# Kernel tuning notes

Measured on AMD Instinct MI355X. Metric: run time of the kernel, lower is better.

## Reference

```python
import jax, jax.numpy as jnp
import numpy as np

EPS = 1e-5

def rmsnorm(x, w, eps=EPS):
    # torch-style RMSNorm: x / rms(x) * weight
    return x * jax.lax.rsqrt(jnp.mean(x * x, axis=-1, keepdims=True) + eps) * w

def setup_inputs() -> dict:
    key = jax.random.key(0)
    k1, k2 = jax.random.split(key)
    B, T, D, Q, K = 8, 1024, 1024, 8, 4096
    d = D // Q
    x = jax.random.normal(k1, (B, T, D), dtype=jnp.float32)
    codebooks = jax.random.normal(k2, (Q, K, d), dtype=jnp.float32)
    input_norm_w = jnp.ones((D,), dtype=jnp.float32)
    output_norm_w = jnp.ones((D,), dtype=jnp.float32)
    return {"x": x, "codebooks": codebooks,
            "input_norm_w": input_norm_w, "output_norm_w": output_norm_w}

def reference(x, codebooks, input_norm_w, output_norm_w):
    B, T, D = x.shape
    Q, K, d = codebooks.shape
    xn = rmsnorm(x, input_norm_w)
    xq = xn.reshape(B, T, Q, d)  # split hidden into Q sub-vectors
    # squared euclidean distances (argmin equal to cdist argmin)
    x2 = jnp.sum(xq * xq, axis=-1, keepdims=True)          # [B,T,Q,1]
    c2 = jnp.sum(codebooks * codebooks, axis=-1)           # [Q,K]
    xc = jnp.einsum('btqd,qkd->btqk', xq, codebooks)       # [B,T,Q,K]
    d2 = x2 - 2.0 * xc + c2[None, None]                    # [B,T,Q,K]
    idx = jnp.argmin(d2, axis=-1)                          # [B,T,Q] int
    # gather nearest code per quantizer: equivalent of stacked embedding lookups
    quant = codebooks[jnp.arange(Q)[None, None, :], idx]   # [B,T,Q,d]
    quant = quant.reshape(B, T, D)
    out = rmsnorm(quant, output_norm_w)
    return out, idx
```

## Files before the change

kernel.cpp:

```cpp
#include <hip/hip_runtime.h>
#include <math.h>
#include <float.h>

#define Q_     8
#define K_     4096
#define dd_    128
#define D_     1024
#define ROWS   8192
#define NCHUNK 64
#define TAU    0.04f

typedef __attribute__((ext_vector_type(8))) _Float16 f16x8;
typedef __attribute__((ext_vector_type(4))) float f32x4;
typedef __attribute__((ext_vector_type(4))) unsigned int u32x4;

typedef const __attribute__((address_space(1))) unsigned int* gas_p;
typedef __attribute__((address_space(3))) unsigned int* las_p;

__device__ inline unsigned f2u(float x) { union { float f; unsigned u; } v; v.f = x; return v.u; }
__device__ inline float u2f(unsigned x) { union { unsigned u; float f; } v; v.u = x; return v.f; }
__device__ inline unsigned short f2h(float x) {
    union { _Float16 h; unsigned short u; } v; v.h = (_Float16)x; return v.u;
}
__device__ inline unsigned umin_(unsigned a, unsigned b) { return a < b ? a : b; }
__device__ inline unsigned umax_(unsigned a, unsigned b) { return a > b ? a : b; }
__device__ inline unsigned fflip(float x) {
    unsigned u = f2u(x);
    return (u & 0x80000000u) ? ~u : (u | 0x80000000u);
}
__device__ inline unsigned long long shfl_xor_u64(unsigned long long v, int m) {
    unsigned lo = (unsigned)v, hi = (unsigned)(v >> 32);
    lo = __shfl_xor(lo, m, 64);
    hi = __shfl_xor(hi, m, 64);
    return ((unsigned long long)hi << 32) | lo;
}
__device__ inline unsigned dec_k(unsigned v, int e) {
    unsigned tg = v & 0x7Fu;
    return ((tg >> 1) << 6) | (((unsigned)e >> 4) << 5) | ((tg & 1u) << 4) | ((unsigned)e & 15u);
}

__global__ void k_prep(const float* __restrict__ cb, const float* __restrict__ x,
                       const float* __restrict__ w, float* __restrict__ xn,
                       unsigned short* __restrict__ panels, float* __restrict__ c2h,
                       float* __restrict__ x2h, int* __restrict__ cntF, int* __restrict__ cntS) {
    const int bid = blockIdx.x, t = threadIdx.x;
    if (bid == 0 && t == 0) { *cntF = 0; *cntS = 0; }
    if (bid < NCHUNK * Q_) {
        int c = bid & 63, q = bid >> 6;
        const float* src = cb + ((size_t)q * K_ + c * 64) * dd_;
        unsigned short* dst = panels + (size_t)(q * NCHUNK + c) * 8192;
        #pragma unroll
        for (int i = 0; i < 4; i++) {
            int sid = i * 256 + t;
            int n = sid >> 4, j = sid & 15;
            const float* sp = src + n * dd_ + j * 8;
            f32x4 v0 = *(const f32x4*)sp;
            f32x4 v1 = *(const f32x4*)(sp + 4);
            float xs[8] = {v0.x, v0.y, v0.z, v0.w, v1.x, v1.y, v1.z, v1.w};
            unsigned short hb[8];
            float ss = 0.0f;
            #pragma unroll
            for (int e = 0; e < 8; e++) {
                float xv = -xs[e];
                ss = fmaf(xv, xv, ss);
                hb[e] = f2h(xv);
            }
            int slot = j ^ (n & 15);
            u32x4 H;
            H.x = (unsigned)hb[0] | ((unsigned)hb[1] << 16);
            H.y = (unsigned)hb[2] | ((unsigned)hb[3] << 16);
            H.z = (unsigned)hb[4] | ((unsigned)hb[5] << 16);
            H.w = (unsigned)hb[6] | ((unsigned)hb[7] << 16);
            *(u32x4*)&dst[(n * 16 + slot) * 8] = H;
            ss += __shfl_xor(ss, 1, 64);
            ss += __shfl_xor(ss, 2, 64);
            ss += __shfl_xor(ss, 4, 64);
            ss += __shfl_xor(ss, 8, 64);
            if (j == 0) c2h[q * K_ + c * 64 + n] = 0.5f * ss;
        }
    } else {
        int row = bid - NCHUNK * Q_;
        const float4 v = *(const float4*)(x + (size_t)row * D_ + t * 4);
        float ss = v.x * v.x + v.y * v.y + v.z * v.z + v.w * v.w;
        #pragma unroll
        for (int o = 32; o > 0; o >>= 1) ss += __shfl_xor(ss, o, 64);
        __shared__ float acc[4];
        if ((t & 63) == 0) acc[t >> 6] = ss;
        __syncthreads();
        float tot = (acc[0] + acc[1]) + (acc[2] + acc[3]);
        float sc  = 1.0f / sqrtf(tot * (1.0f / D_) + 1e-5f);
        const float4 wv = *(const float4*)(w + t * 4);
        float4 o;
        o.x = v.x * sc * wv.x; o.y = v.y * sc * wv.y;
        o.z = v.z * sc * wv.z; o.w = v.w * sc * wv.w;
        *(float4*)(xn + (size_t)row * D_ + t * 4) = o;
        float so = o.x * o.x + o.y * o.y + o.z * o.z + o.w * o.w;
        so += __shfl_xor(so, 1, 64);
        so += __shfl_xor(so, 2, 64);
        so += __shfl_xor(so, 4, 64);
        so += __shfl_xor(so, 8, 64);
        so += __shfl_xor(so, 16, 64);
        if ((t & 31) == 0) x2h[row * Q_ + (t >> 5)] = 0.5f * so;
    }
}

#define STAGE(CN) do {                                                                   \
    const char* src_ = (const char*)(panels + panq + (size_t)(CN) * 8192);               \
    char* stg_ = smem + ((CN) & 1) * 16384;                                              \
    _Pragma("unroll")                                                                    \
    for (int i_ = 0; i_ < 4; i_++) {                                                     \
        int boff_ = i_ * 4096 + t * 16;                                                  \
        __builtin_amdgcn_global_load_lds((gas_p)(src_ + boff_), (las_p)(stg_ + boff_),   \
                                         16, 0, 0);                                      \
    }                                                                                    \
} while (0)

__launch_bounds__(256, 4)
__global__ void k_dist(const float* __restrict__ xn, const unsigned short* __restrict__ panels,
                       const float* __restrict__ c2h, const float* __restrict__ x2h,
                       int* __restrict__ idxi, float* __restrict__ idxf,
                       int* __restrict__ listF, int* __restrict__ cntF,
                       int* __restrict__ srl, int* __restrict__ cntS,
                       unsigned long long* __restrict__ resc,
                       unsigned char* __restrict__ fbm) {
    __shared__ char smem[32768];

    const int t    = threadIdx.x;
    const int lane = t & 63, wave = t >> 6;
    const int wm = wave >> 1, wn = wave & 1;
    const int col = lane & 15, quad = lane >> 4;
    const int q = blockIdx.y;
    const int row0 = blockIdx.x * 64;

    f16x8 ah[2][4];
    #pragma unroll
    for (int mt = 0; mt < 2; mt++) {
        #pragma unroll
        for (int kt = 0; kt < 4; kt++) {
            const float* ap = xn + (size_t)(row0 + wm * 32 + mt * 16 + col) * D_
                              + q * dd_ + kt * 32 + quad * 8;
            f32x4 v0 = *(const f32x4*)ap;
            f32x4 v1 = *(const f32x4*)(ap + 4);
            #pragma unroll
            for (int e = 0; e < 8; e++) {
                float xv = (e < 4) ? v0[e] : v1[e - 4];
                ah[mt][kt][e] = (_Float16)xv;
            }
        }
    }

    f32x4 x2v[2];
    #pragma unroll
    for (int mt = 0; mt < 2; mt++)
        #pragma unroll
        for (int r = 0; r < 4; r++)
            x2v[mt][r] = x2h[(size_t)(row0 + wm * 32 + mt * 16 + quad * 4 + r) * Q_ + q];

    unsigned m1[8], m2[8], m3[8];
    #pragma unroll
    for (int i = 0; i < 8; i++) { m1[i] = 0xFFFFFFFFu; m2[i] = 0xFFFFFFFFu; m3[i] = 0xFFFFFFFFu; }

    const size_t panq = (size_t)q * NCHUNK * 8192;
    const float* c2hq = c2h + q * K_;

    STAGE(0);
    float ch0 = c2hq[wn * 32 + col];
    float ch1 = c2hq[wn * 32 + col + 16];

    for (int c = 0; c < NCHUNK; c++) {
        __syncthreads();
        if (c + 1 < NCHUNK) STAGE(c + 1);
        float ch0n = 0.0f, ch1n = 0.0f;
        if (c + 1 < NCHUNK) {
            ch0n = c2hq[(c + 1) * 64 + wn * 32 + col];
            ch1n = c2hq[(c + 1) * 64 + wn * 32 + col + 16];
        }
        const char* cbuf = smem + (c & 1) * 16384;

        f32x4 acc[2][2];
        #pragma unroll
        for (int mt = 0; mt < 2; mt++) {
            acc[mt][0] = x2v[mt] + ch0;
            acc[mt][1] = x2v[mt] + ch1;
        }

        #pragma unroll
        for (int kt = 0; kt < 4; kt++) {
            const int sw = ((quad + kt * 4) ^ col) * 16;
            const int a0 = (wn * 32 + col) * 256 + sw;
            const int a1 = a0 + 4096;
            f16x8 b0 = *(const f16x8*)(cbuf + a0);
            f16x8 b1 = *(const f16x8*)(cbuf + a1);
            #pragma unroll
            for (int mt = 0; mt < 2; mt++) {
                acc[mt][0] = __builtin_amdgcn_mfma_f32_16x16x32_f16(ah[mt][kt], b0, acc[mt][0], 0, 0, 0);
                acc[mt][1] = __builtin_amdgcn_mfma_f32_16x16x32_f16(ah[mt][kt], b1, acc[mt][1], 0, 0, 0);
            }
        }

        const unsigned tg0 = (unsigned)(c << 1), tg1 = tg0 | 1u;
        #pragma unroll
        for (int mt = 0; mt < 2; mt++) {
            #pragma unroll
            for (int r = 0; r < 4; r++) {
                const int sl = mt * 4 + r;
                unsigned p0 = (f2u(acc[mt][0][r]) & 0xFFFFFF80u) | tg0;
                unsigned p1 = (f2u(acc[mt][1][r]) & 0xFFFFFF80u) | tg1;
                unsigned pmin = umin_(p0, p1), pmax = umax_(p0, p1);
                unsigned a1m = umax_(m1[sl], pmin);
                unsigned a2m = umin_(m2[sl], pmax);
                unsigned a4m = umax_(m2[sl], pmax);
                m1[sl] = umin_(m1[sl], pmin);
                m2[sl] = umin_(a1m, a2m);
                unsigned a3m = umax_(a1m, a2m);
                m3[sl] = umin_(umin_(a3m, a4m), m3[sl]);
            }
        }
        ch0 = ch0n; ch1 = ch1n;
    }

    __syncthreads();
    unsigned* rm1 = (unsigned*)smem;
    unsigned* rm2 = (unsigned*)(smem + 8448);
    unsigned* rm3 = (unsigned*)(smem + 16896);
    #pragma unroll
    for (int mt = 0; mt < 2; mt++) {
        #pragma unroll
        for (int r = 0; r < 4; r++) {
            int sl = mt * 4 + r;
            int row_l = wm * 32 + mt * 16 + quad * 4 + r;
            int e = wn * 16 + col;
            rm1[row_l * 33 + e] = m1[sl];
            rm2[row_l * 33 + e] = m2[sl];
            rm3[row_l * 33 + e] = m3[sl];
        }
    }
    __syncthreads();
    if (t < 64) {
        unsigned b1 = 0xFFFFFFFFu;
        int be = 0;
        for (int e = 0; e < 32; e++) {
            unsigned v1 = rm1[t * 33 + e];
            if (v1 < b1) { b1 = v1; be = e; }
        }
        float thr = u2f(b1 & 0xFFFFFF80u) + TAU;
        int ns = 0, fb = 0;
        unsigned long long candpack = 0;
        for (int e = 0; e < 32; e++) {
            unsigned v1 = rm1[t * 33 + e];
            unsigned v2 = rm2[t * 33 + e];
            unsigned v3 = rm3[t * 33 + e];
            if (u2f(v3 & 0xFFFFFF80u) < thr) fb = 1;
            if (e != be && u2f(v1 & 0xFFFFFF80u) < thr) {
                if (ns < 5) candpack |= (unsigned long long)dec_k(v1, e) << (12 * ns);
                ns++;
            }
            if (u2f(v2 & 0xFFFFFF80u) < thr) {
                if (ns < 5) candpack |= (unsigned long long)dec_k(v2, e) << (12 * ns);
                ns++;
            }
        }
        if (ns > 5) fb = 1;
        unsigned k1 = dec_k(b1, be);
        int item = (row0 + t) * Q_ + q;
        idxi[item] = (int)k1;
        idxf[item] = (float)k1;
        fbm[item] = (unsigned char)fb;
        if (fb) {
            resc[item] = 0xFFFFFFFFFFFFFFFFull;
            int p = atomicAdd(cntF, 1);
            listF[p] = item;
        } else if (ns > 0) {
            int p = atomicAdd(cntS, 1);
            int* e8 = srl + (size_t)p * 8;
            e8[0] = item; e8[1] = ns + 1; e8[2] = (int)k1;
            for (int i = 0; i < ns; i++)
                e8[3 + i] = (int)((candpack >> (12 * i)) & 0xFFFu);
        }
    }
}

__global__ void k_rescue(const float* __restrict__ xn, const float* __restrict__ cb,
                         const float* __restrict__ c2h, const int* __restrict__ listF,
                         const int* __restrict__ cntF, const int* __restrict__ srl,
                         const int* __restrict__ cntS,
                         unsigned long long* __restrict__ resc,
                         int* __restrict__ idxi, float* __restrict__ idxf) {
    __shared__ float xq[dd_];
    __shared__ unsigned long long kshare[8];
    const int t = threadIdx.x;
    if (blockIdx.x < 2048) {
        const int n = *cntF;
        const int seg = blockIdx.x & 7;
        for (int ii = blockIdx.x >> 3; ii < n; ii += 256) {
            __syncthreads();
            int item = listF[ii];
            int rg = item >> 3, q = item & 7;
            if (t < dd_) xq[t] = xn[(size_t)rg * D_ + q * dd_ + t];
            __syncthreads();
            unsigned long long best = 0xFFFFFFFFFFFFFFFFull;
            #pragma unroll
            for (int i = 0; i < 2; i++) {
                int k = seg * 512 + i * 256 + t;
                const float* cp = cb + ((size_t)q * K_ + k) * dd_;
                float dot = 0.0f;
                #pragma unroll 8
                for (int d = 0; d < dd_; d += 4) {
                    f32x4 cv = *(const f32x4*)(cp + d);
                    dot = fmaf(cv.x, xq[d],     dot);
                    dot = fmaf(cv.y, xq[d + 1], dot);
                    dot = fmaf(cv.z, xq[d + 2], dot);
                    dot = fmaf(cv.w, xq[d + 3], dot);
                }
                float s = c2h[q * K_ + k] - dot;
                unsigned long long key = ((unsigned long long)fflip(s) << 32) | (unsigned)k;
                best = best < key ? best : key;
            }
            #pragma unroll
            for (int o = 32; o > 0; o >>= 1) {
                unsigned long long other = shfl_xor_u64(best, o);
                best = best < other ? best : other;
            }
            if ((t & 63) == 0) kshare[t >> 6] = best;
            __syncthreads();
            if (t == 0) {
                unsigned long long b = kshare[0];
                b = b < kshare[1] ? b : kshare[1];
                b = b < kshare[2] ? b : kshare[2];
                b = b < kshare[3] ? b : kshare[3];
                atomicMin(&resc[item], b);
            }
        }
    } else {
        const int n = *cntS;
        for (int ii = (int)blockIdx.x - 2048; ii < n; ii += 2048) {
            __syncthreads();
            const int* e = srl + (size_t)ii * 8;
            int item = e[0], nc = e[1];
            int rg = item >> 3, q = item & 7;
            if (t < dd_) xq[t] = xn[(size_t)rg * D_ + q * dd_ + t];
            __syncthreads();
            int g = t >> 5, l = t & 31;
            unsigned long long key = 0xFFFFFFFFFFFFFFFFull;
            if (g < nc) {
                int k = e[2 + g];
                const float* cp = cb + ((size_t)q * K_ + k) * dd_ + l * 4;
                f32x4 cv = *(const f32x4*)cp;
                float dot = cv.x * xq[l * 4]     + cv.y * xq[l * 4 + 1]
                          + cv.z * xq[l * 4 + 2] + cv.w * xq[l * 4 + 3];
                dot += __shfl_xor(dot, 16, 64);
                dot += __shfl_xor(dot, 8, 64);
                dot += __shfl_xor(dot, 4, 64);
                dot += __shfl_xor(dot, 2, 64);
                dot += __shfl_xor(dot, 1, 64);
                float s = c2h[q * K_ + k] - dot;
                key = ((unsigned long long)fflip(s) << 32) | (unsigned)k;
            }
            if (l == 0) kshare[g] = key;
            __syncthreads();
            if (t == 0) {
                unsigned long long b = kshare[0];
                #pragma unroll
                for (int gg = 1; gg < 8; gg++) b = b < kshare[gg] ? b : kshare[gg];
                int k = (int)(unsigned)(b & 0xFFFFFFFFull);
                idxi[item] = k;
                idxf[item] = (float)k;
            }
        }
    }
}

__global__ void k_out(const float* __restrict__ cb, const int* __restrict__ idx_i,
                      const unsigned long long* __restrict__ resc,
                      const unsigned char* __restrict__ fbm,
                      const float* __restrict__ w, float* __restrict__ out,
                      float* __restrict__ idxf) {
    int row = blockIdx.x;
    int t   = threadIdx.x;
    __shared__ int   sidx[Q_];
    __shared__ float acc[4];
    if (t < Q_) {
        int item = row * Q_ + t;
        int k = idx_i[item];
        if (fbm[item]) {
            k = (int)(unsigned)(resc[item] & 0xFFFFFFFFull);
            idxf[item] = (float)k;
        }
        sidx[t] = k;
    }
    __syncthreads();
    int col = t * 4;
    int q   = col >> 7;
    int dc  = col & 127;
    const float4 v = *(const float4*)(cb + ((size_t)q * K_ + sidx[q]) * dd_ + dc);
    float ss = v.x * v.x + v.y * v.y + v.z * v.z + v.w * v.w;
    #pragma unroll
    for (int o = 32; o > 0; o >>= 1) ss += __shfl_xor(ss, o, 64);
    if ((t & 63) == 0) acc[t >> 6] = ss;
    __syncthreads();
    float tot = (acc[0] + acc[1]) + (acc[2] + acc[3]);
    float sc  = 1.0f / sqrtf(tot * (1.0f / D_) + 1e-5f);
    const float4 wv = *(const float4*)(w + col);
    float4 o;
    o.x = v.x * sc * wv.x; o.y = v.y * sc * wv.y;
    o.z = v.z * sc * wv.z; o.w = v.w * sc * wv.w;
    *(float4*)(out + (size_t)row * D_ + col) = o;
}

extern "C" void kernel_launch(void* const* d_in, const int* in_sizes, int n_in,
                              void* d_out, int out_size, void* d_ws, size_t ws_size,
                              hipStream_t stream) {
    const float* x     = (const float*)d_in[0];
    const float* cb    = (const float*)d_in[1];
    const float* w_in  = (const float*)d_in[2];
    const float* w_out = (const float*)d_in[3];

    float* out  = (float*)d_out;
    float* idxf = out + (size_t)ROWS * D_;

    unsigned short* panels = (unsigned short*)d_ws;
    float* c2h  = (float*)((char*)d_ws + (8u << 20));
    float* x2h  = c2h + Q_ * K_;
    unsigned long long* resc = (unsigned long long*)(x2h + (size_t)ROWS * Q_);
    int*   idxi = (int*)(resc + (size_t)ROWS * Q_);
    int*   listF = idxi + ROWS * Q_;
    int*   srl  = listF + ROWS * Q_;
    unsigned char* fbm = (unsigned char*)(srl + (size_t)ROWS * Q_ * 8);
    int*   cntF = (int*)(fbm + ROWS * Q_);
    int*   cntS = cntF + 1;

    k_prep  <<<dim3(NCHUNK * Q_ + ROWS), 256, 0, stream>>>(cb, x, w_in, out, panels, c2h, x2h, cntF, cntS);
    k_dist  <<<dim3(ROWS / 64, Q_),      256, 0, stream>>>(out, panels, c2h, x2h, idxi, idxf, listF, cntF, srl, cntS, resc, fbm);
    k_rescue<<<dim3(4096),               256, 0, stream>>>(out, cb, c2h, listF, cntF, srl, cntS, resc, idxi, idxf);
    k_out   <<<dim3(ROWS),               256, 0, stream>>>(cb, idxi, resc, fbm, w_out, out, idxf);
}
```

Baseline: 217.0 us.

## Give each wave its own LDS double buffer and drop block barriers in distance loop

Restructures the distance kernel's main loop. Previously all four waves shared a block-wide double buffer of 64-code chunks and hit a __syncthreads every iteration. Now each wave stages its own 16-code half-chunk into a private LDS region and waits on it with explicit s_waitcnt vmcnt, so block-level barriers go away. Chunks become 32 codes, which doubles the iteration count and adjusts the tag encoding, and the top-3 update is simplified to one candidate per step. The cost is that waves sharing a column half each load the same panel data, so global/L2 traffic doubles, and correctness depends on the hand-written vmcnt count.

```diff
diff --git a/kernel.cpp b/kernel.cpp
--- a/kernel.cpp
+++ b/kernel.cpp
@@ -7,7 +7,7 @@
 #define dd_    128
 #define D_     1024
 #define ROWS   8192
-#define NCHUNK 64
+#define NCHUNK 128
 #define TAU    0.04f
 
 typedef __attribute__((ext_vector_type(8))) _Float16 f16x8;
@@ -35,8 +35,7 @@
     return ((unsigned long long)hi << 32) | lo;
 }
 __device__ inline unsigned dec_k(unsigned v, int e) {
-    unsigned tg = v & 0x7Fu;
-    return ((tg >> 1) << 6) | (((unsigned)e >> 4) << 5) | ((tg & 1u) << 4) | ((unsigned)e & 15u);
+    return (v & 0x7Fu) * 32u + (unsigned)e;
 }
 
 __global__ void k_prep(const float* __restrict__ cb, const float* __restrict__ x,
@@ -45,10 +44,10 @@
                        float* __restrict__ x2h, int* __restrict__ cntF, int* __restrict__ cntS) {
     const int bid = blockIdx.x, t = threadIdx.x;
     if (bid == 0 && t == 0) { *cntF = 0; *cntS = 0; }
-    if (bid < NCHUNK * Q_) {
+    if (bid < 64 * Q_) {
         int c = bid & 63, q = bid >> 6;
         const float* src = cb + ((size_t)q * K_ + c * 64) * dd_;
-        unsigned short* dst = panels + (size_t)(q * NCHUNK + c) * 8192;
+        unsigned short* dst = panels + ((size_t)q * 64 + c) * 8192;
         #pragma unroll
         for (int i = 0; i < 4; i++) {
             int sid = i * 256 + t;
@@ -79,7 +78,7 @@
             if (j == 0) c2h[q * K_ + c * 64 + n] = 0.5f * ss;
         }
     } else {
-        int row = bid - NCHUNK * Q_;
+        int row = bid - 64 * Q_;
         const float4 v = *(const float4*)(x + (size_t)row * D_ + t * 4);
         float ss = v.x * v.x + v.y * v.y + v.z * v.z + v.w * v.w;
         #pragma unroll
@@ -104,14 +103,42 @@
     }
 }
 
-#define STAGE(CN) do {                                                                   \
-    const char* src_ = (const char*)(panels + panq + (size_t)(CN) * 8192);               \
-    char* stg_ = smem + ((CN) & 1) * 16384;                                              \
+#define ITER(C, CHCUR, CHNXT) do {                                                       \
+    if ((C) + 1 < NCHUNK) {                                                              \
+        const char* s_ = (const char*)(panels + panq + (size_t)((C) + 1) * 4096)         \
+                         + wn * 4096;                                                    \
+        char* d_ = mybuf + (((C) + 1) & 1) * 4096;                                       \
+        _Pragma("unroll")                                                                \
+        for (int i_ = 0; i_ < 4; i_++) {                                                 \
+            int o_ = i_ * 1024 + lane * 16;                                              \
+            __builtin_amdgcn_global_load_lds((gas_p)(s_ + o_), (las_p)(d_ + o_),         \
+                                             16, 0, 0);                                  \
+        }                                                                                \
+        CHNXT = c2hq[((C) + 1) * 32 + wn * 16 + col];                                    \
+        asm volatile("s_waitcnt vmcnt(5)" ::: "memory");                                 \
+    } else {                                                                             \
+        asm volatile("s_waitcnt vmcnt(0)" ::: "memory");                                 \
+    }                                                                                    \
+    const char* cb_ = mybuf + ((C) & 1) * 4096;                                          \
+    f32x4 acc0 = x2v0 + (CHCUR);                                                         \
+    f32x4 acc1 = x2v1 + (CHCUR);                                                         \
     _Pragma("unroll")                                                                    \
-    for (int i_ = 0; i_ < 4; i_++) {                                                     \
-        int boff_ = i_ * 4096 + t * 16;                                                  \
-        __builtin_amdgcn_global_load_lds((gas_p)(src_ + boff_), (las_p)(stg_ + boff_),   \
-                                         16, 0, 0);                                      \
+    for (int kt_ = 0; kt_ < 4; kt_++) {                                                  \
+        f16x8 b_ = *(const f16x8*)(cb_ + col * 256 + (((quad + kt_ * 4) ^ col) * 16));   \
+        acc0 = __builtin_amdgcn_mfma_f32_16x16x32_f16(ah[0][kt_], b_, acc0, 0, 0, 0);    \
+        acc1 = __builtin_amdgcn_mfma_f32_16x16x32_f16(ah[1][kt_], b_, acc1, 0, 0, 0);    \
+    }                                                                                    \
+    const unsigned tg_ = (unsigned)(C);                                                  \
+    _Pragma("unroll")                                                                    \
+    for (int r_ = 0; r_ < 4; r_++) {                                                     \
+        unsigned p0_ = (f2u(acc0[r_]) & 0xFFFFFF80u) | tg_;                              \
+        unsigned n3_ = umin_(m3[r_], umax_(m2[r_], p0_));                                \
+        unsigned n2_ = umax_(m1[r_], umin_(m2[r_], p0_));                                \
+        m1[r_] = umin_(m1[r_], p0_); m2[r_] = n2_; m3[r_] = n3_;                         \
+        unsigned p1_ = (f2u(acc1[r_]) & 0xFFFFFF80u) | tg_;                              \
+        unsigned n3b_ = umin_(m3[4 + r_], umax_(m2[4 + r_], p1_));                       \
+        unsigned n2b_ = umax_(m1[4 + r_], umin_(m2[4 + r_], p1_));                       \
+        m1[4 + r_] = umin_(m1[4 + r_], p1_); m2[4 + r_] = n2b_; m3[4 + r_] = n3b_;       \
     }                                                                                    \
 } while (0)
 
@@ -131,6 +158,8 @@
     const int col = lane & 15, quad = lane >> 4;
     const int q = blockIdx.y;
     const int row0 = blockIdx.x * 64;
+
+    char* mybuf = smem + wave * 8192;
 
     f16x8 ah[2][4];
     #pragma unroll
@@ -149,74 +178,34 @@
         }
     }
 
-    f32x4 x2v[2];
+    f32x4 x2v0, x2v1;
     #pragma unroll
-    for (int mt = 0; mt < 2; mt++)
-        #pragma unroll
-        for (int r = 0; r < 4; r++)
-            x2v[mt][r] = x2h[(size_t)(row0 + wm * 32 + mt * 16 + quad * 4 + r) * Q_ + q];
+    for (int r = 0; r < 4; r++) {
+        x2v0[r] = x2h[(size_t)(row0 + wm * 32 + quad * 4 + r) * Q_ + q];
+        x2v1[r] = x2h[(size_t)(row0 + wm * 32 + 16 + quad * 4 + r) * Q_ + q];
+    }
 
     unsigned m1[8], m2[8], m3[8];
     #pragma unroll
     for (int i = 0; i < 8; i++) { m1[i] = 0xFFFFFFFFu; m2[i] = 0xFFFFFFFFu; m3[i] = 0xFFFFFFFFu; }
 
-    const size_t panq = (size_t)q * NCHUNK * 8192;
+    const size_t panq = (size_t)q * (NCHUNK * 4096);
     const float* c2hq = c2h + q * K_;
 
-    STAGE(0);
-    float ch0 = c2hq[wn * 32 + col];
-    float ch1 = c2hq[wn * 32 + col + 16];
-
-    for (int c = 0; c < NCHUNK; c++) {
-        __syncthreads();
-        if (c + 1 < NCHUNK) STAGE(c + 1);
-        float ch0n = 0.0f, ch1n = 0.0f;
-        if (c + 1 < NCHUNK) {
-            ch0n = c2hq[(c + 1) * 64 + wn * 32 + col];
-            ch1n = c2hq[(c + 1) * 64 + wn * 32 + col + 16];
-        }
-        const char* cbuf = smem + (c & 1) * 16384;
-
-        f32x4 acc[2][2];
+    float chA, chB;
+    {
+        const char* s0 = (const char*)(panels + panq) + wn * 4096;
         #pragma unroll
-        for (int mt = 0; mt < 2; mt++) {
-            acc[mt][0] = x2v[mt] + ch0;
-            acc[mt][1] = x2v[mt] + ch1;
-        }
-
-        #pragma unroll
-        for (int kt = 0; kt < 4; kt++) {
-            const int sw = ((quad + kt * 4) ^ col) * 16;
-            const int a0 = (wn * 32 + col) * 256 + sw;
-            const int a1 = a0 + 4096;
-            f16x8 b0 = *(const f16x8*)(cbuf + a0);
-            f16x8 b1 = *(const f16x8*)(cbuf + a1);
-            #pragma unroll
-            for (int mt = 0; mt < 2; mt++) {
-                acc[mt][0] = __builtin_amdgcn_mfma_f32_16x16x32_f16(ah[mt][kt], b0, acc[mt][0], 0, 0, 0);
-                acc[mt][1] = __builtin_amdgcn_mfma_f32_16x16x32_f16(ah[mt][kt], b1, acc[mt][1], 0, 0, 0);
-            }
-        }
-
-        const unsigned tg0 = (unsigned)(c << 1), tg1 = tg0 | 1u;
-        #pragma unroll
-        for (int mt = 0; mt < 2; mt++) {
-            #pragma unroll
-            for (int r = 0; r < 4; r++) {
-                const int sl = mt * 4 + r;
-                unsigned p0 = (f2u(acc[mt][0][r]) & 0xFFFFFF80u) | tg0;
-                unsigned p1 = (f2u(acc[mt][1][r]) & 0xFFFFFF80u) | tg1;
-                unsigned pmin = umin_(p0, p1), pmax = umax_(p0, p1);
-                unsigned a1m = umax_(m1[sl], pmin);
-                unsigned a2m = umin_(m2[sl], pmax);
-                unsigned a4m = umax_(m2[sl], pmax);
-                m1[sl] = umin_(m1[sl], pmin);
-                m2[sl] = umin_(a1m, a2m);
-                unsigned a3m = umax_(a1m, a2m);
-                m3[sl] = umin_(umin_(a3m, a4m), m3[sl]);
-            }
-        }
-        ch0 = ch0n; ch1 = ch1n;
+        for (int i = 0; i < 4; i++) {
+            int o = i * 1024 + lane * 16;
+            __builtin_amdgcn_global_load_lds((gas_p)(s0 + o), (las_p)(mybuf + o), 16, 0, 0);
+        }
+        chA = c2hq[wn * 16 + col];
+    }
+
+    for (int c = 0; c < NCHUNK; c += 2) {
+        ITER(c,     chA, chB);
+        ITER(c + 1, chB, chA);
     }
 
     __syncthreads();
@@ -429,8 +418,8 @@
     int*   cntF = (int*)(fbm + ROWS * Q_);
     int*   cntS = cntF + 1;
 
-    k_prep  <<<dim3(NCHUNK * Q_ + ROWS), 256, 0, stream>>>(cb, x, w_in, out, panels, c2h, x2h, cntF, cntS);
-    k_dist  <<<dim3(ROWS / 64, Q_),      256, 0, stream>>>(out, panels, c2h, x2h, idxi, idxf, listF, cntF, srl, cntS, resc, fbm);
-    k_rescue<<<dim3(4096),               256, 0, stream>>>(out, cb, c2h, listF, cntF, srl, cntS, resc, idxi, idxf);
-    k_out   <<<dim3(ROWS),               256, 0, stream>>>(cb, idxi, resc, fbm, w_out, out, idxf);
-}
+    k_prep  <<<dim3(64 * Q_ + ROWS), 256, 0, stream>>>(cb, x, w_in, out, panels, c2h, x2h, cntF, cntS);
+    k_dist  <<<dim3(ROWS / 64, Q_),  256, 0, stream>>>(out, panels, c2h, x2h, idxi, idxf, listF, cntF, srl, cntS, resc, fbm);
+    k_rescue<<<dim3(4096),           256, 0, stream>>>(out, cb, c2h, listF, cntF, srl, cntS, resc, idxi, idxf);
+    k_out   <<<dim3(ROWS),           256, 0, stream>>>(cb, idxi, resc, fbm, w_out, out, idxf);
+}
```

New measurement: 234.1 us. +7.9%, slower.
